# Kernel optimization log

Measured on AMD Instinct MI355X. Metric: run time of the kernel, lower is better.

Reference implementation:

```python
import jax, jax.numpy as jnp
import numpy as np

N = 50000      # nodes
E = 800000     # edges (avg degree 16)
DIM = 128      # in_dim == out_dim
H = 8          # num_heads
D = DIM // H   # per-head dim = 16


def layer_norm(x, g, b, eps=1e-5):
    m = x.mean(-1, keepdims=True)
    v = ((x - m) ** 2).mean(-1, keepdims=True)
    return (x - m) / jnp.sqrt(v + eps) * g + b


def setup_inputs() -> dict:
    key = jax.random.key(0)
    ks = jax.random.split(key, 16)
    w = 0.02
    return {
        "x": jax.random.normal(ks[0], (N, DIM), dtype=jnp.float32),
        "src": jax.random.randint(ks[1], (E,), 0, N),
        "dst": jax.random.randint(ks[2], (E,), 0, N),
        "Wq": jax.random.normal(ks[3], (DIM, DIM), dtype=jnp.float32) * w,
        "bq": jnp.zeros((DIM,), dtype=jnp.float32),
        "Wk": jax.random.normal(ks[4], (DIM, DIM), dtype=jnp.float32) * w,
        "bk": jnp.zeros((DIM,), dtype=jnp.float32),
        "Wv": jax.random.normal(ks[5], (DIM, DIM), dtype=jnp.float32) * w,
        "bv": jnp.zeros((DIM,), dtype=jnp.float32),
        "Wo": jax.random.normal(ks[6], (DIM, DIM), dtype=jnp.float32) * w,
        "bo": jnp.zeros((DIM,), dtype=jnp.float32),
        "ln1_g": jnp.ones((DIM,), dtype=jnp.float32),
        "ln1_b": jnp.zeros((DIM,), dtype=jnp.float32),
        "ln2_g": jnp.ones((DIM,), dtype=jnp.float32),
        "ln2_b": jnp.zeros((DIM,), dtype=jnp.float32),
    }


def reference(x, src, dst, Wq, bq, Wk, bk, Wv, bv, Wo, bo, ln1_g, ln1_b, ln2_g, ln2_b):
    # Q/K/V projections, split into heads: [N, H, D]
    Q = (x @ Wq + bq).reshape(N, H, D)
    K = (x @ Wk + bk).reshape(N, H, D)
    V = (x @ Wv + bv).reshape(N, H, D)

    # per-edge src_dot_dst: (K[src] * Q[dst]).sum(-1) -> [E, H, 1]
    score = (K[src] * Q[dst]).sum(-1, keepdims=True)
    # scaled_exp with clamp(-5, 5)
    score = jnp.exp(jnp.clip(score / np.sqrt(D).astype(np.float32), -5.0, 5.0))

    # scatter-sum of V[src] * score into dst nodes -> wV [N, H, D]
    wV = jax.ops.segment_sum(V[src] * score, dst, num_segments=N)
    # (the original also computes z = segment_sum(score) but never uses it)

    # residual + LayerNorm
    h = x + wV.reshape(N, DIM)
    h = layer_norm(h, ln1_g, ln1_b)

    # sublayer wrapper: h + relu(O(norm(h)))  (dropout=0)
    h = h + jax.nn.relu(layer_norm(h, ln2_g, ln2_b) @ Wo + bo)
    return h
```

## Files before the change

### kernel.cpp

```cpp
#include <hip/hip_runtime.h>
#include <hip/hip_bf16.h>

#define N_NODES 50000
#define N_EDGES 800000
#define DIM     128
#define CAP     96
#define PREP_BLOCKS 258

typedef __attribute__((ext_vector_type(8))) short bf16x8;
typedef __attribute__((ext_vector_type(4))) float f32x4;
typedef __fp16 f16;
typedef __attribute__((ext_vector_type(2))) __fp16 f16x2;

__device__ __forceinline__ unsigned short f2bf(float f) {
    union { float f; unsigned u; } c; c.f = f;
    unsigned r = c.u + 0x7fffu + ((c.u >> 16) & 1u);
    return (unsigned short)(r >> 16);
}
__device__ __forceinline__ float bfhi(unsigned int u) {
    union { unsigned int u; float f; } c; c.u = u & 0xffff0000u; return c.f;
}
__device__ __forceinline__ float bflo(unsigned int u) {
    union { unsigned int u; float f; } c; c.u = u << 16; return c.f;
}
__device__ __forceinline__ float bfs(unsigned short s) {
    union { unsigned int u; float f; } c; c.u = (unsigned)s << 16; return c.f;
}
__device__ __forceinline__ void unpack8(uint4 w, float* f) {
    f[0] = bflo(w.x); f[1] = bfhi(w.x);
    f[2] = bflo(w.y); f[3] = bfhi(w.y);
    f[4] = bflo(w.z); f[5] = bfhi(w.z);
    f[6] = bflo(w.w); f[7] = bfhi(w.w);
}

__global__ __launch_bounds__(256) void prep_fill_kernel(
    const float* __restrict__ Wq, const float* __restrict__ Wk,
    const float* __restrict__ Wv, const float* __restrict__ Wo,
    const float* __restrict__ bq, const float* __restrict__ bk,
    const float* __restrict__ bv,
    const int* __restrict__ src, const int* __restrict__ dst,
    unsigned short* __restrict__ WT, unsigned short* __restrict__ WoT,
    float* __restrict__ bqkv,
    int* __restrict__ counts, unsigned short* __restrict__ bucket)
{
    if (blockIdx.x < PREP_BLOCKS) {
        const int t = blockIdx.x * 256 + threadIdx.x;
        if (t < 384 * 128) {
            int j = t >> 7, k = t & 127;
            int which = j >> 7, jj = j & 127;
            const float* W = which == 0 ? Wq : which == 1 ? Wk : Wv;
            WT[t] = f2bf(W[k * 128 + jj]);
        } else if (t < 384 * 128 + 128 * 128) {
            int t2 = t - 384 * 128;
            int j = t2 >> 7, k = t2 & 127;
            WoT[t2] = f2bf(Wo[k * 128 + j]);
        } else if (t < 384 * 128 + 128 * 128 + 384) {
            int j = t - (384 * 128 + 128 * 128);
            bqkv[j] = j < 128 ? bq[j] : j < 256 ? bk[j - 128] : bv[j - 256];
        }
    } else {
        const int e = (blockIdx.x - PREP_BLOCKS) * 256 + threadIdx.x;
        if (e >= N_EDGES) return;
        const int s = src[e];
        const int d = dst[e];
        const int pos = atomicAdd(&counts[d], 1);
        if (pos < CAP) bucket[(unsigned)d * CAP + pos] = (unsigned short)s;
    }
}

__global__ __launch_bounds__(256) void qkv_mfma(
    const float* __restrict__ x, const unsigned short* __restrict__ WT,
    const float* __restrict__ bqkv,
    unsigned short* __restrict__ Q, unsigned char* __restrict__ K8,
    unsigned short* __restrict__ Vh )
{
    __shared__ union {
        unsigned short xs[32][136];
        unsigned short cs[32][384];
    } sh;

    const int w   = threadIdx.x >> 6;
    const int l   = threadIdx.x & 63;
    const int l15 = l & 15;
    const int lk  = l >> 4;
    const int n0  = blockIdx.x * 32;

    for (int idx = threadIdx.x; idx < 32 * 32; idx += 256) {
        const int row = idx >> 5, c4 = idx & 31;
        const int node = n0 + row;
        unsigned short s0 = 0, s1 = 0, s2 = 0, s3 = 0;
        if (node < N_NODES) {
            float4 f = ((const float4*)(x + (size_t)node * 128))[c4];
            s0 = f2bf(f.x); s1 = f2bf(f.y); s2 = f2bf(f.z); s3 = f2bf(f.w);
        }
        unsigned short* p = &sh.xs[row][c4 * 4];
        p[0] = s0; p[1] = s1; p[2] = s2; p[3] = s3;
    }
    __syncthreads();

    f32x4 acc[6][2];
#pragma unroll
    for (int t = 0; t < 6; ++t)
#pragma unroll
        for (int rg = 0; rg < 2; ++rg) acc[t][rg] = (f32x4){0.f, 0.f, 0.f, 0.f};

#pragma unroll
    for (int kk = 0; kk < 4; ++kk) {
        const int kb = kk * 32 + lk * 8;
        bf16x8 a[2];
#pragma unroll
        for (int rg = 0; rg < 2; ++rg)
            a[rg] = *(const bf16x8*)(&sh.xs[rg * 16 + l15][kb]);
#pragma unroll
        for (int t = 0; t < 6; ++t) {
            const int j0 = w * 96 + t * 16;
            bf16x8 b = *(const bf16x8*)(WT + (size_t)(j0 + l15) * 128 + kb);
            acc[t][0] = __builtin_amdgcn_mfma_f32_16x16x32_bf16(a[0], b, acc[t][0], 0, 0, 0);
            acc[t][1] = __builtin_amdgcn_mfma_f32_16x16x32_bf16(a[1], b, acc[t][1], 0, 0, 0);
        }
    }
    __syncthreads();

#pragma unroll
    for (int t = 0; t < 6; ++t) {
        const int j = w * 96 + t * 16 + l15;
        const float bias = bqkv[j];
#pragma unroll
        for (int rg = 0; rg < 2; ++rg)
#pragma unroll
            for (int r = 0; r < 4; ++r)
                sh.cs[rg * 16 + lk * 4 + r][j] = f2bf(acc[t][rg][r] + bias);
    }
    __syncthreads();

    for (int idx = threadIdx.x; idx < 32 * 16; idx += 256) {
        const int row = idx >> 4, c8 = idx & 15;
        const int node = n0 + row;
        if (node < N_NODES)
            *(uint4*)(Q + (size_t)node * 128 + c8 * 8) =
                ((const uint4*)&sh.cs[row][0])[c8];
    }
    for (int idx = threadIdx.x; idx < 32 * 16; idx += 256) {
        const int row = idx >> 4, c8 = idx & 15;
        const int node = n0 + row;
        if (node < N_NODES) {
            const unsigned short* p = &sh.cs[row][128 + c8 * 8];
            int w0 = __builtin_amdgcn_cvt_pk_fp8_f32(bfs(p[0]), bfs(p[1]), 0, false);
            w0     = __builtin_amdgcn_cvt_pk_fp8_f32(bfs(p[2]), bfs(p[3]), w0, true);
            int w1 = __builtin_amdgcn_cvt_pk_fp8_f32(bfs(p[4]), bfs(p[5]), 0, false);
            w1     = __builtin_amdgcn_cvt_pk_fp8_f32(bfs(p[6]), bfs(p[7]), w1, true);
            *(uint2*)(K8 + (size_t)node * 128 + c8 * 8) =
                make_uint2((unsigned)w0, (unsigned)w1);
        }
    }
    for (int idx = threadIdx.x; idx < 32 * 16; idx += 256) {
        const int row = idx >> 4, c8 = idx & 15;
        const int node = n0 + row;
        if (node < N_NODES) {
            const unsigned short* p = &sh.cs[row][256 + c8 * 8];
            union { uint4 u; f16x2 h[4]; } vv;
            vv.h[0] = __builtin_amdgcn_cvt_pkrtz(bfs(p[0]), bfs(p[1]));
            vv.h[1] = __builtin_amdgcn_cvt_pkrtz(bfs(p[2]), bfs(p[3]));
            vv.h[2] = __builtin_amdgcn_cvt_pkrtz(bfs(p[4]), bfs(p[5]));
            vv.h[3] = __builtin_amdgcn_cvt_pkrtz(bfs(p[6]), bfs(p[7]));
            *(uint4*)(Vh + (size_t)node * 128 + c8 * 8) = vv.u;
        }
    }
}

__device__ __forceinline__ void edge_accum(uint2 kw, uint4 vw,
                                           const float* q, f16x2* acc2)
{
    float kf[8];
#if __has_builtin(__builtin_amdgcn_cvt_pk_f32_fp8)
    {
        auto p0 = __builtin_amdgcn_cvt_pk_f32_fp8((int)kw.x, false);
        auto p1 = __builtin_amdgcn_cvt_pk_f32_fp8((int)kw.x, true);
        auto p2 = __builtin_amdgcn_cvt_pk_f32_fp8((int)kw.y, false);
        auto p3 = __builtin_amdgcn_cvt_pk_f32_fp8((int)kw.y, true);
        kf[0] = p0[0]; kf[1] = p0[1]; kf[2] = p1[0]; kf[3] = p1[1];
        kf[4] = p2[0]; kf[5] = p2[1]; kf[6] = p3[0]; kf[7] = p3[1];
    }
#else
    kf[0] = __builtin_amdgcn_cvt_f32_fp8(kw.x, 0);
    kf[1] = __builtin_amdgcn_cvt_f32_fp8(kw.x, 1);
    kf[2] = __builtin_amdgcn_cvt_f32_fp8(kw.x, 2);
    kf[3] = __builtin_amdgcn_cvt_f32_fp8(kw.x, 3);
    kf[4] = __builtin_amdgcn_cvt_f32_fp8(kw.y, 0);
    kf[5] = __builtin_amdgcn_cvt_f32_fp8(kw.y, 1);
    kf[6] = __builtin_amdgcn_cvt_f32_fp8(kw.y, 2);
    kf[7] = __builtin_amdgcn_cvt_f32_fp8(kw.y, 3);
#endif
    float dot = q[0]*kf[0] + q[1]*kf[1] + q[2]*kf[2] + q[3]*kf[3]
              + q[4]*kf[4] + q[5]*kf[5] + q[6]*kf[6] + q[7]*kf[7];
    dot += __shfl_xor(dot, 1);
    float z = fminf(fmaxf(dot * 0.25f, -5.f), 5.f);
    float sc = __expf(z);
    f16x2 sc2 = __builtin_amdgcn_cvt_pkrtz(sc, sc);
    union { uint4 u; f16x2 h[4]; } v; v.u = vw;
#pragma unroll
    for (int j = 0; j < 4; ++j)
        acc2[j] = __builtin_elementwise_fma(v.h[j], sc2, acc2[j]);
}

__global__ __launch_bounds__(256) void gather_ln_kernel(
    const float* __restrict__ x,
    const unsigned short* __restrict__ Qb, const unsigned char* __restrict__ K8,
    const unsigned short* __restrict__ Vh,
    const int* __restrict__ counts, const unsigned short* __restrict__ bucket,
    const float* __restrict__ g1, const float* __restrict__ b1,
    unsigned short* __restrict__ h )
{
    const int node = blockIdx.x * 4 + (threadIdx.x >> 6);
    if (node >= N_NODES) return;
    const unsigned lane = threadIdx.x & 15;
    const unsigned grp  = (threadIdx.x >> 4) & 3;

    const uint4* Q4 = (const uint4*)Qb;
    const uint2* K2 = (const uint2*)K8;
    const uint4* V4 = (const uint4*)Vh;

    const float4* x4 = (const float4*)(x + (size_t)node * DIM);
    const float4 xa = x4[lane * 2], xb = x4[lane * 2 + 1];

    float q[8];
    unpack8(Q4[(unsigned)node * 16u + lane], q);

    int cnt = counts[node];
    if (cnt > CAP) cnt = CAP;
    const unsigned base = (unsigned)node * CAP;

    f16x2 acc2[4];
#pragma unroll
    for (int j = 0; j < 4; ++j) acc2[j] = (f16x2){(f16)0.f, (f16)0.f};

    int i = grp;
    for (; i + 4 < cnt; i += 8) {
        const unsigned s0 = bucket[base + i];
        const unsigned s1 = bucket[base + i + 4];
        const uint2 kw0 = K2[s0 * 16u + lane];
        const uint4 vw0 = V4[s0 * 16u + lane];
        const uint2 kw1 = K2[s1 * 16u + lane];
        const uint4 vw1 = V4[s1 * 16u + lane];
        edge_accum(kw0, vw0, q, acc2);
        edge_accum(kw1, vw1, q, acc2);
    }
    if (i < cnt) {
        const unsigned s0 = bucket[base + i];
        const uint2 kw0 = K2[s0 * 16u + lane];
        const uint4 vw0 = V4[s0 * 16u + lane];
        edge_accum(kw0, vw0, q, acc2);
    }

#pragma unroll
    for (int j = 0; j < 4; ++j) {
        float t = __builtin_bit_cast(float, acc2[j]);
        t = __shfl_xor(t, 16);
        acc2[j] += __builtin_bit_cast(f16x2, t);
        t = __builtin_bit_cast(float, acc2[j]);
        t = __shfl_xor(t, 32);
        acc2[j] += __builtin_bit_cast(f16x2, t);
    }
    float wv[8];
#pragma unroll
    for (int j = 0; j < 4; ++j) {
        wv[2 * j]     = (float)acc2[j][0];
        wv[2 * j + 1] = (float)acc2[j][1];
    }

    float a[8] = { xa.x + wv[0], xa.y + wv[1], xa.z + wv[2], xa.w + wv[3],
                   xb.x + wv[4], xb.y + wv[5], xb.z + wv[6], xb.w + wv[7] };

    float sum = 0.f;
#pragma unroll
    for (int j = 0; j < 8; ++j) sum += a[j];
#pragma unroll
    for (int m = 1; m < 16; m <<= 1) sum += __shfl_xor(sum, m);
    float mean = sum * (1.f / 128.f);
    float vs = 0.f;
#pragma unroll
    for (int j = 0; j < 8; ++j) { a[j] -= mean; vs += a[j] * a[j]; }
#pragma unroll
    for (int m = 1; m < 16; m <<= 1) vs += __shfl_xor(vs, m);
    float rstd = rsqrtf(vs * (1.f / 128.f) + 1e-5f);

    if ((threadIdx.x & 63) < 16) {
        const float4 g1a = ((const float4*)g1)[lane * 2], g1b = ((const float4*)g1)[lane * 2 + 1];
        const float4 b1a = ((const float4*)b1)[lane * 2], b1b = ((const float4*)b1)[lane * 2 + 1];
        float hv[8];
        hv[0] = a[0] * rstd * g1a.x + b1a.x;  hv[1] = a[1] * rstd * g1a.y + b1a.y;
        hv[2] = a[2] * rstd * g1a.z + b1a.z;  hv[3] = a[3] * rstd * g1a.w + b1a.w;
        hv[4] = a[4] * rstd * g1b.x + b1b.x;  hv[5] = a[5] * rstd * g1b.y + b1b.y;
        hv[6] = a[6] * rstd * g1b.z + b1b.z;  hv[7] = a[7] * rstd * g1b.w + b1b.w;

        uint4 up;
        up.x = (unsigned)f2bf(hv[0]) | ((unsigned)f2bf(hv[1]) << 16);
        up.y = (unsigned)f2bf(hv[2]) | ((unsigned)f2bf(hv[3]) << 16);
        up.z = (unsigned)f2bf(hv[4]) | ((unsigned)f2bf(hv[5]) << 16);
        up.w = (unsigned)f2bf(hv[6]) | ((unsigned)f2bf(hv[7]) << 16);
        ((uint4*)(h + (size_t)node * DIM))[lane] = up;
    }
}

__global__ __launch_bounds__(256) void out_mfma(
    const unsigned short* __restrict__ h, const unsigned short* __restrict__ WoT,
    const float* __restrict__ g2, const float* __restrict__ b2,
    const float* __restrict__ bo, float* __restrict__ out)
{
    __shared__ unsigned short hs[32][136];
    __shared__ union {
        unsigned short us[32][136];
        float ls[32][128];
    } shB;

    const int w   = threadIdx.x >> 6;
    const int l   = threadIdx.x & 63;
    const int l15 = l & 15;
    const int lk  = l >> 4;
    const int n0  = blockIdx.x * 32;

    for (int idx = threadIdx.x; idx < 32 * 16; idx += 256) {
        const int row = idx >> 4, c8 = idx & 15;
        const int node = n0 + row;
        uint4 v = make_uint4(0, 0, 0, 0);
        if (node < N_NODES)
            v = ((const uint4*)(h + (size_t)node * 128))[c8];
        *(uint4*)(&hs[row][c8 * 8]) = v;
    }
    __syncthreads();

    {
        const int row = threadIdx.x >> 3;
        const int sub = threadIdx.x & 7;
        float v[16];
#pragma unroll
        for (int j = 0; j < 16; ++j) v[j] = bfs(hs[row][sub * 16 + j]);
        float sum = 0.f;
#pragma unroll
        for (int j = 0; j < 16; ++j) sum += v[j];
#pragma unroll
        for (int m = 1; m < 8; m <<= 1) sum += __shfl_xor(sum, m);
        float mean = sum * (1.f / 128.f);
        float vs = 0.f;
#pragma unroll
        for (int j = 0; j < 16; ++j) { v[j] -= mean; vs += v[j] * v[j]; }
#pragma unroll
        for (int m = 1; m < 8; m <<= 1) vs += __shfl_xor(vs, m);
        float rstd = rsqrtf(vs * (1.f / 128.f) + 1e-5f);
#pragma unroll
        for (int j4 = 0; j4 < 4; ++j4) {
            const float4 gg = ((const float4*)g2)[sub * 4 + j4];
            const float4 bb = ((const float4*)b2)[sub * 4 + j4];
            shB.us[row][sub * 16 + j4 * 4 + 0] = f2bf(v[j4 * 4 + 0] * rstd * gg.x + bb.x);
            shB.us[row][sub * 16 + j4 * 4 + 1] = f2bf(v[j4 * 4 + 1] * rstd * gg.y + bb.y);
            shB.us[row][sub * 16 + j4 * 4 + 2] = f2bf(v[j4 * 4 + 2] * rstd * gg.z + bb.z);
            shB.us[row][sub * 16 + j4 * 4 + 3] = f2bf(v[j4 * 4 + 3] * rstd * gg.w + bb.w);
        }
    }
    __syncthreads();

    f32x4 acc[2][2];
#pragma unroll
    for (int t = 0; t < 2; ++t)
#pragma unroll
        for (int rg = 0; rg < 2; ++rg) acc[t][rg] = (f32x4){0.f, 0.f, 0.f, 0.f};

#pragma unroll
    for (int kk = 0; kk < 4; ++kk) {
        const int kb = kk * 32 + lk * 8;
        bf16x8 a[2];
#pragma unroll
        for (int rg = 0; rg < 2; ++rg)
            a[rg] = *(const bf16x8*)(&shB.us[rg * 16 + l15][kb]);
#pragma unroll
        for (int t = 0; t < 2; ++t) {
            const int j0 = w * 32 + t * 16;
            bf16x8 b = *(const bf16x8*)(WoT + (size_t)(j0 + l15) * 128 + kb);
            acc[t][0] = __builtin_amdgcn_mfma_f32_16x16x32_bf16(a[0], b, acc[t][0], 0, 0, 0);
            acc[t][1] = __builtin_amdgcn_mfma_f32_16x16x32_bf16(a[1], b, acc[t][1], 0, 0, 0);
        }
    }
    __syncthreads();

#pragma unroll
    for (int t = 0; t < 2; ++t) {
        const int j = w * 32 + t * 16 + l15;
        const float bias = bo[j];
#pragma unroll
        for (int rg = 0; rg < 2; ++rg)
#pragma unroll
            for (int r = 0; r < 4; ++r)
                shB.ls[rg * 16 + lk * 4 + r][j] = fmaxf(acc[t][rg][r] + bias, 0.f);
    }
    __syncthreads();

    for (int idx = threadIdx.x; idx < 32 * 32; idx += 256) {
        const int row = idx >> 5, c4 = idx & 31;
        const int node = n0 + row;
        if (node < N_NODES) {
            float4 v = ((const float4*)shB.ls[row])[c4];
            const unsigned short* hp = &hs[row][c4 * 4];
            ((float4*)(out + (size_t)node * 128))[c4] = make_float4(
                bfs(hp[0]) + v.x, bfs(hp[1]) + v.y,
                bfs(hp[2]) + v.z, bfs(hp[3]) + v.w);
        }
    }
}

extern "C" void kernel_launch(void* const* d_in, const int* in_sizes, int n_in,
                              void* d_out, int out_size, void* d_ws, size_t ws_size,
                              hipStream_t stream)
{
    const float* x    = (const float*)d_in[0];
    const int*   src  = (const int*)  d_in[1];
    const int*   dst  = (const int*)  d_in[2];
    const float* Wq   = (const float*)d_in[3];
    const float* bq   = (const float*)d_in[4];
    const float* Wk   = (const float*)d_in[5];
    const float* bk   = (const float*)d_in[6];
    const float* Wv   = (const float*)d_in[7];
    const float* bv   = (const float*)d_in[8];
    const float* Wo   = (const float*)d_in[9];
    const float* bo   = (const float*)d_in[10];
    const float* ln1g = (const float*)d_in[11];
    const float* ln1b = (const float*)d_in[12];
    const float* ln2g = (const float*)d_in[13];
    const float* ln2b = (const float*)d_in[14];

    float* out = (float*)d_out;
    char*  wsb = (char*)d_ws;

    const size_t NM = (size_t)N_NODES * DIM;
    unsigned short* Qb = (unsigned short*)(wsb);
    unsigned short* Vh = Qb + NM;
    unsigned short* hb = Vh + NM;
    unsigned char*  K8 = (unsigned char*)(hb + NM);
    unsigned short* WT  = (unsigned short*)(K8 + NM);
    unsigned short* WoT = WT + 384 * 128;
    float* bqkv   = (float*)(WoT + 128 * 128);
    int*   counts = (int*)(bqkv + 384);
    unsigned short* bucket = (unsigned short*)(counts + N_NODES);

    hipMemsetAsync(counts, 0, N_NODES * sizeof(int), stream);

    prep_fill_kernel<<<PREP_BLOCKS + (N_EDGES + 255) / 256, 256, 0, stream>>>(
        Wq, Wk, Wv, Wo, bq, bk, bv, src, dst,
        WT, WoT, bqkv, counts, bucket);

    qkv_mfma<<<(N_NODES + 31) / 32, 256, 0, stream>>>(
        x, WT, bqkv, Qb, K8, Vh);

    gather_ln_kernel<<<(N_NODES + 3) / 4, 256, 0, stream>>>(
        x, Qb, K8, Vh, counts, bucket, ln1g, ln1b, hb);

    out_mfma<<<(N_NODES + 31) / 32, 256, 0, stream>>>(
        hb, WoT, ln2g, ln2b, bo, out);
}
```

Before: 154.2 us.

## Fuse edge bucket fill into QKV kernel and pad atomic counters

Moves the per-edge atomic bucket fill out of the weight-prep kernel and into the QKV projection launch as extra blocks, so the atomic scatter overlaps with the MFMA projection work. The counts memset is folded into the prep kernel, and each counter is padded to a 64-byte stride to reduce atomic contention and false sharing. This removes one memset launch and lets the memory-bound fill run alongside the compute-bound GEMM. In exchange, the counts array grows sixteenfold and each counter read in the gather is a strided access.

```diff
diff --git a/kernel.cpp b/kernel.cpp
--- a/kernel.cpp
+++ b/kernel.cpp
@@ -6,6 +6,8 @@
 #define DIM     128
 #define CAP     96
 #define PREP_BLOCKS 258
+#define QKV_BLOCKS  1563
+#define FILL_BLOCKS 3125
 
 typedef __attribute__((ext_vector_type(8))) short bf16x8;
 typedef __attribute__((ext_vector_type(4))) float f32x4;
@@ -33,44 +35,36 @@
     f[6] = bflo(w.w); f[7] = bfhi(w.w);
 }
 
-__global__ __launch_bounds__(256) void prep_fill_kernel(
+__global__ __launch_bounds__(256) void prep_kernel(
     const float* __restrict__ Wq, const float* __restrict__ Wk,
     const float* __restrict__ Wv, const float* __restrict__ Wo,
     const float* __restrict__ bq, const float* __restrict__ bk,
     const float* __restrict__ bv,
-    const int* __restrict__ src, const int* __restrict__ dst,
     unsigned short* __restrict__ WT, unsigned short* __restrict__ WoT,
-    float* __restrict__ bqkv,
-    int* __restrict__ counts, unsigned short* __restrict__ bucket)
-{
-    if (blockIdx.x < PREP_BLOCKS) {
-        const int t = blockIdx.x * 256 + threadIdx.x;
-        if (t < 384 * 128) {
-            int j = t >> 7, k = t & 127;
-            int which = j >> 7, jj = j & 127;
-            const float* W = which == 0 ? Wq : which == 1 ? Wk : Wv;
-            WT[t] = f2bf(W[k * 128 + jj]);
-        } else if (t < 384 * 128 + 128 * 128) {
-            int t2 = t - 384 * 128;
-            int j = t2 >> 7, k = t2 & 127;
-            WoT[t2] = f2bf(Wo[k * 128 + j]);
-        } else if (t < 384 * 128 + 128 * 128 + 384) {
-            int j = t - (384 * 128 + 128 * 128);
-            bqkv[j] = j < 128 ? bq[j] : j < 256 ? bk[j - 128] : bv[j - 256];
-        }
-    } else {
-        const int e = (blockIdx.x - PREP_BLOCKS) * 256 + threadIdx.x;
-        if (e >= N_EDGES) return;
-        const int s = src[e];
-        const int d = dst[e];
-        const int pos = atomicAdd(&counts[d], 1);
-        if (pos < CAP) bucket[(unsigned)d * CAP + pos] = (unsigned short)s;
-    }
-}
-
-__global__ __launch_bounds__(256) void qkv_mfma(
+    float* __restrict__ bqkv, int* __restrict__ counts)
+{
+    const int t = blockIdx.x * 256 + threadIdx.x;
+    if (t < N_NODES) counts[(unsigned)t << 4] = 0;
+    if (t < 384 * 128) {
+        int j = t >> 7, k = t & 127;
+        int which = j >> 7, jj = j & 127;
+        const float* W = which == 0 ? Wq : which == 1 ? Wk : Wv;
+        WT[t] = f2bf(W[k * 128 + jj]);
+    } else if (t < 384 * 128 + 128 * 128) {
+        int t2 = t - 384 * 128;
+        int j = t2 >> 7, k = t2 & 127;
+        WoT[t2] = f2bf(Wo[k * 128 + j]);
+    } else if (t < 384 * 128 + 128 * 128 + 384) {
+        int j = t - (384 * 128 + 128 * 128);
+        bqkv[j] = j < 128 ? bq[j] : j < 256 ? bk[j - 128] : bv[j - 256];
+    }
+}
+
+__global__ __launch_bounds__(256) void qkv_fill_kernel(
     const float* __restrict__ x, const unsigned short* __restrict__ WT,
     const float* __restrict__ bqkv,
+    const int* __restrict__ src, const int* __restrict__ dst,
+    int* __restrict__ counts, unsigned short* __restrict__ bucket,
     unsigned short* __restrict__ Q, unsigned char* __restrict__ K8,
     unsigned short* __restrict__ Vh )
 {
@@ -78,6 +72,16 @@
         unsigned short xs[32][136];
         unsigned short cs[32][384];
     } sh;
+
+    if (blockIdx.x >= QKV_BLOCKS) {
+        const int e = (blockIdx.x - QKV_BLOCKS) * 256 + threadIdx.x;
+        if (e >= N_EDGES) return;
+        const int s = src[e];
+        const int d = dst[e];
+        const int pos = atomicAdd(&counts[(unsigned)d << 4], 1);
+        if (pos < CAP) bucket[(unsigned)d * CAP + pos] = (unsigned short)s;
+        return;
+    }
 
     const int w   = threadIdx.x >> 6;
     const int l   = threadIdx.x & 63;
@@ -226,7 +230,7 @@
     float q[8];
     unpack8(Q4[(unsigned)node * 16u + lane], q);
 
-    int cnt = counts[node];
+    int cnt = counts[(unsigned)node << 4];
     if (cnt > CAP) cnt = CAP;
     const unsigned base = (unsigned)node * CAP;
 
@@ -439,16 +443,13 @@
     unsigned short* WoT = WT + 384 * 128;
     float* bqkv   = (float*)(WoT + 128 * 128);
     int*   counts = (int*)(bqkv + 384);
-    unsigned short* bucket = (unsigned short*)(counts + N_NODES);
-
-    hipMemsetAsync(counts, 0, N_NODES * sizeof(int), stream);
-
-    prep_fill_kernel<<<PREP_BLOCKS + (N_EDGES + 255) / 256, 256, 0, stream>>>(
-        Wq, Wk, Wv, Wo, bq, bk, bv, src, dst,
-        WT, WoT, bqkv, counts, bucket);
-
-    qkv_mfma<<<(N_NODES + 31) / 32, 256, 0, stream>>>(
-        x, WT, bqkv, Qb, K8, Vh);
+    unsigned short* bucket = (unsigned short*)(counts + (size_t)N_NODES * 16);
+
+    prep_kernel<<<PREP_BLOCKS, 256, 0, stream>>>(
+        Wq, Wk, Wv, Wo, bq, bk, bv, WT, WoT, bqkv, counts);
+
+    qkv_fill_kernel<<<QKV_BLOCKS + FILL_BLOCKS, 256, 0, stream>>>(
+        x, WT, bqkv, src, dst, counts, bucket, Qb, K8, Vh);
 
     gather_ln_kernel<<<(N_NODES + 3) / 4, 256, 0, stream>>>(
         x, Qb, K8, Vh, counts, bucket, ln1g, ln1b, hb);
```

Measured after the change: 164.1 us. 1.06x slower.
